# Performance work log

Hardware: AMD Instinct MI355X
Metric: run time of the kernel (lower is better)

The kernel has to match this reference:

```python
import jax, jax.numpy as jnp
import numpy as np

C = 60                 # channels
WINDOW_SIZES = [4, 8, 12]
SHIFTS = 4
BN_EPS = 1e-5


def setup_inputs() -> dict:
    key = jax.random.key(0)
    ks = jax.random.split(key, 4)
    s = 0.05
    return {
        "x": jax.random.normal(ks[0], (8, C, 288, 288), dtype=jnp.float32),
        # project_inp: Conv2d(C, 2C, k=1) + BatchNorm2d(2C) (inference form)
        "W_in": jax.random.normal(ks[1], (2 * C, C), dtype=jnp.float32) * s,
        "b_in": jnp.zeros((2 * C,), dtype=jnp.float32),
        "bn_gamma": jnp.ones((2 * C,), dtype=jnp.float32),
        "bn_beta": jnp.zeros((2 * C,), dtype=jnp.float32),
        "bn_mean": jax.random.normal(ks[2], (2 * C,), dtype=jnp.float32) * s,
        "bn_var": jnp.ones((2 * C,), dtype=jnp.float32),
        # project_out: Conv2d(C, C, k=1)
        "W_out": jax.random.normal(ks[3], (C, C), dtype=jnp.float32) * s,
        "b_out": jnp.zeros((C,), dtype=jnp.float32),
    }


def _window_self_attn(x_, wsize, shift):
    """One GMSA branch: roll -> window partition -> QQ^T softmax V -> merge -> unroll.
    x_ : [b, 2c, H, W] where first c channels are q, last c are v."""
    b, c2, H, W = x_.shape
    c = c2 // 2
    if shift > 0:
        x_ = jnp.roll(x_, shift=(-(wsize // 2), -(wsize // 2)), axis=(2, 3))
    nh, nw = H // wsize, W // wsize
    # 'b (qv c) (h dh) (w dw) -> qv (b h w) (dh dw) c'
    xw = x_.reshape(b, 2, c, nh, wsize, nw, wsize)
    xw = xw.transpose(1, 0, 3, 5, 4, 6, 2).reshape(2, b * nh * nw, wsize * wsize, c)
    q, v = xw[0], xw[1]                      # [n, p, c] with p = wsize*wsize
    atn = jax.nn.softmax(jnp.einsum("npc,nqc->npq", q, q), axis=-1)
    y = jnp.einsum("npq,nqc->npc", atn, v)
    # '(b h w) (dh dw) c -> b c (h dh) (w dw)'
    y = y.reshape(b, nh, nw, wsize, wsize, c).transpose(0, 5, 1, 3, 2, 4)
    y = y.reshape(b, c, H, W)
    if shift > 0:
        y = jnp.roll(y, shift=(wsize // 2, wsize // 2), axis=(2, 3))
    return y, atn


def reference(x, W_in, b_in, bn_gamma, bn_beta, bn_mean, bn_var, W_out, b_out):
    # 1x1 conv = channel matmul, then inference BatchNorm
    xp = jnp.einsum("oc,bchw->bohw", W_in, x) + b_in[None, :, None, None]
    inv = bn_gamma / jnp.sqrt(bn_var + BN_EPS)
    xp = xp * inv[None, :, None, None] + (bn_beta - bn_mean * inv)[None, :, None, None]
    split = 2 * C // 3  # = 40 per branch (q,v interleaved as 2x20)
    ys, atns = [], []
    off = 0
    for ws in WINDOW_SIZES:
        y_, a_ = _window_self_attn(xp[:, off:off + split], ws, SHIFTS)
        off += split
        ys.append(y_)
        atns.append(a_)
    y = jnp.concatenate(ys, axis=1)  # [b, C, H, W]
    y = jnp.einsum("oc,bchw->bohw", W_out, y) + b_out[None, :, None, None]
    return (y, atns[0], atns[1], atns[2])
```

## Files before the change

kernel.cpp:

```cpp
#include <hip/hip_runtime.h>


constexpr int HW = 288 * 288;
constexpr long long ATN0_OFF = 39813120LL;
constexpr long long ATN1_OFF = ATN0_OFF + 41472LL * 256;
constexpr long long ATN2_OFF = ATN1_OFF + 10368LL * 4096;

constexpr size_t YB_OFF = 0;
constexpr size_t WP_OFF = 79626240;
constexpr size_t BP_OFF = WP_OFF + 28800;
constexpr size_t XP_OFF = BP_OFF + 512;

typedef __attribute__((ext_vector_type(8))) short  bf16x8;
typedef __attribute__((ext_vector_type(4))) short  bf16x4;
typedef __attribute__((ext_vector_type(4))) float  f32x4;

__device__ __forceinline__ unsigned bfrnd(float f) {
    unsigned u = __float_as_uint(f);
    return (u + 0x7fffu + ((u >> 16) & 1u)) >> 16;
}
__device__ __forceinline__ unsigned bfpack(float a, float b) { return bfrnd(a) | (bfrnd(b) << 16); }

#if defined(__has_builtin)
#if __has_builtin(__builtin_amdgcn_mfma_f32_16x16x16bf16_1k)
#define HAVE_MFMA16 1
#endif
#endif

__device__ __forceinline__ f32x4 mfma16(bf16x4 a, bf16x4 b, f32x4 c) {
#ifdef HAVE_MFMA16
    return __builtin_amdgcn_mfma_f32_16x16x16bf16_1k(a, b, c, 0, 0, 0);
#else
    f32x4 d;
    asm("v_mfma_f32_16x16x16_bf16 %0, %1, %2, %3" : "=v"(d) : "v"(a), "v"(b), "v"(c));
    return d;
#endif
}

__device__ __forceinline__ f32x4 mfma32(bf16x8 a, bf16x8 b, f32x4 c) {
    return __builtin_amdgcn_mfma_f32_16x16x32_bf16(a, b, c, 0, 0, 0);
}

__global__ void prep_kernel(const float* __restrict__ W_in, const float* __restrict__ b_in,
                            const float* __restrict__ gamma, const float* __restrict__ beta,
                            const float* __restrict__ mean, const float* __restrict__ var,
                            float* __restrict__ Wp, float* __restrict__ bp) {
    int o = threadIdx.x;
    if (o < 120) {
        float inv = gamma[o] / sqrtf(var[o] + 1e-5f);
        for (int c = 0; c < 60; ++c) Wp[o * 60 + c] = W_in[o * 60 + c] * inv;
        bp[o] = b_in[o] * inv + beta[o] - mean[o] * inv;
    } else if (o < 128) {
        bp[o] = 0.f;
    }
}

__global__ __launch_bounds__(256, 3) void proj_in_kernel(const float* __restrict__ x,
                                                         const float* __restrict__ Wp,
                                                         const float* __restrict__ bp,
                                                         unsigned short* __restrict__ xp) {
    __shared__ __align__(16) unsigned short wq[128 * 64];
    __shared__ __align__(16) unsigned short ys[128 * 120];

    const int tid = threadIdx.x;
    const long long pixel0 = (long long)blockIdx.x * 128;
    const int b   = (int)(pixel0 / HW);
    const int hw0 = (int)(pixel0 % HW);

    for (int i = tid; i < 8192; i += 256) {
        const int row = i >> 6, ch = i & 63;
        wq[i] = (row < 120 && ch < 60) ? (unsigned short)bfrnd(Wp[row * 60 + ch]) : (unsigned short)0;
    }

    const int wave = tid >> 6, lane = tid & 63, lo = lane & 15, g = lane >> 4;

    uint4 xlo[2], xhi[2];
    #pragma unroll
    for (int mt2 = 0; mt2 < 2; ++mt2) {
        const int row = (wave * 2 + mt2) * 16 + lo;
        const float* xb = x + (long long)b * 60 * HW + hw0 + row;
        unsigned short tl[8], th[8];
        #pragma unroll
        for (int e = 0; e < 8; ++e) {
            const int cl = g * 8 + e;
            tl[e] = (unsigned short)bfrnd(xb[(long long)cl * HW]);
            const int ch = 32 + g * 8 + e;
            th[e] = (ch < 60) ? (unsigned short)bfrnd(xb[(long long)ch * HW]) : (unsigned short)0;
        }
        xlo[mt2] = *reinterpret_cast<const uint4*>(tl);
        xhi[mt2] = *reinterpret_cast<const uint4*>(th);
    }
    __syncthreads();

    #pragma unroll
    for (int n = 0; n < 8; ++n) {
        uint4 wfl = *reinterpret_cast<const uint4*>(&wq[(n * 16 + lo) * 64 + g * 8]);
        uint4 wfh = *reinterpret_cast<const uint4*>(&wq[(n * 16 + lo) * 64 + 32 + g * 8]);
        const int oc0 = n * 16 + 4 * g;
        const f32x4 bpv = *reinterpret_cast<const f32x4*>(&bp[oc0]);
        #pragma unroll
        for (int mt2 = 0; mt2 < 2; ++mt2) {
            f32x4 z = {0.f, 0.f, 0.f, 0.f};
            f32x4 acc = mfma32(*reinterpret_cast<bf16x8*>(&wfl),
                               *reinterpret_cast<bf16x8*>(&xlo[mt2]), z);
            acc = mfma32(*reinterpret_cast<bf16x8*>(&wfh),
                         *reinterpret_cast<bf16x8*>(&xhi[mt2]), acc);
            if (oc0 < 120) {
                const int pixel = (wave * 2 + mt2) * 16 + lo;
                uint2 t;
                t.x = bfpack(acc[0] + bpv[0], acc[1] + bpv[1]);
                t.y = bfpack(acc[2] + bpv[2], acc[3] + bpv[3]);
                *reinterpret_cast<uint2*>(&ys[pixel * 120 + oc0]) = t;
            }
        }
    }
    __syncthreads();

    for (int i = tid; i < 3 * 1280; i += 256) {
        const int br = i / 1280, j = i - br * 1280, p = j / 10, c = j - p * 10;
        const uint2 v = *reinterpret_cast<const uint2*>(&ys[p * 120 + br * 40 + c * 4]);
        reinterpret_cast<uint2*>(xp + ((long long)(b * 3 + br) * HW + hw0) * 40)[p * 10 + c] = v;
    }
}

template <int WS, int NWIN, int BLOCK, int WPW, int BRANCH, int MINW>
__launch_bounds__(BLOCK, MINW)
__global__ void branch_kernel(const unsigned short* __restrict__ xp,
                              unsigned short* __restrict__ ybuf,
                              float* __restrict__ atn) {
    constexpr int P    = WS * WS;
    constexpr int RT   = P / 16;
    constexpr int SH   = WS / 2;
    constexpr int NWND = 288 / WS;
    constexpr int RSTR = 56;
    constexpr int WAVES = BLOCK / 64;
    constexpr int WINS_PER_WAVE = (NWIN * WPW) / WAVES;

    __shared__ __align__(16) unsigned short qv[NWIN * P * RSTR];
    __shared__ __align__(16) unsigned short ys[NWIN * P * 20];

    const int tid = threadIdx.x;
    const int w0 = blockIdx.x * NWIN;

    for (int idx = tid; idx < NWIN * P * 5; idx += BLOCK) {
        const int wl  = idx / (P * 5);
        const int rem = idx - wl * (P * 5);
        const int pix = rem / 5;
        const int ck  = rem - pix * 5;
        const int w   = w0 + wl;
        const int b   = w / (NWND * NWND);
        const int r2  = w - b * (NWND * NWND);
        const int wi  = r2 / NWND;
        const int wj  = r2 - wi * NWND;
        const int gh  = (wi * WS + pix / WS + SH) % 288;
        const int gw  = (wj * WS + pix % WS + SH) % 288;
        const uint4 d = *reinterpret_cast<const uint4*>(
            xp + ((long long)(b * 3 + BRANCH) * HW + gh * 288 + gw) * 40 + ck * 8);
        *reinterpret_cast<uint4*>(&qv[(wl * P + pix) * RSTR + ck * 8]) = d;
    }
    __syncthreads();

    const int wave = tid >> 6;
    const int lane = tid & 63;
    const int lo   = lane & 15;
    const int g    = lane >> 4;

    for (int wk = 0; wk < WINS_PER_WAVE; ++wk) {
        const int wl   = (WPW == 1) ? (wave * WINS_PER_WAVE + wk) : (wave >> 1);
        const int half = (WPW == 1) ? 0 : (wave & 1);
        const int w    = w0 + wl;
        const unsigned short* wbase = qv + wl * P * RSTR;

        bf16x8 F[RT];
        #pragma unroll
        for (int t = 0; t < RT; ++t) {
            uint4 u = *reinterpret_cast<const uint4*>(&wbase[(16 * t + lo) * RSTR + g * 8]);
            if (g == 2) { u.z = 0; u.w = 0; }
            if (g == 3) { u.x = 0; u.y = 0; u.z = 0; u.w = 0; }
            F[t] = *reinterpret_cast<bf16x8*>(&u);
        }

        bf16x4 VB[RT][2];
        #pragma unroll
        for (int i = 0; i < RT; ++i) {
            #pragma unroll
            for (int ct = 0; ct < 2; ++ct) {
                const int c = ct * 16 + lo;
                bf16x4 vv;
                #pragma unroll
                for (int jj = 0; jj < 4; ++jj) {
                    const int row = 16 * i + 4 * g + jj;
                    vv[jj] = (c < 20) ? (short)wbase[row * RSTR + 20 + c] : (short)0;
                }
                VB[i][ct] = vv;
            }
        }

        const int jstart = (WPW == 1) ? 0 : (half * ((RT + 1) / 2));
        const int jend   = (WPW == 1) ? RT : ((half == 0) ? ((RT + 1) / 2) : RT);
        for (int j = jstart; j < jend; ++j) {
            f32x4 S[RT];
            #pragma unroll
            for (int i = 0; i < RT; ++i) {
                f32x4 z = {0.f, 0.f, 0.f, 0.f};
                S[i] = mfma32(F[i], F[j], z);
            }

            float m = S[0][0];
            #pragma unroll
            for (int i = 0; i < RT; ++i) {
                #pragma unroll
                for (int r = 0; r < 4; ++r) m = fmaxf(m, S[i][r]);
            }
            m = fmaxf(m, __shfl_xor(m, 16));
            m = fmaxf(m, __shfl_xor(m, 32));
            float sum = 0.f;
            #pragma unroll
            for (int i = 0; i < RT; ++i) {
                #pragma unroll
                for (int r = 0; r < 4; ++r) { float e = __expf(S[i][r] - m); S[i][r] = e; sum += e; }
            }
            sum += __shfl_xor(sum, 16);
            sum += __shfl_xor(sum, 32);
            const float inv = 1.0f / sum;
            #pragma unroll
            for (int i = 0; i < RT; ++i) {
                S[i][0] *= inv; S[i][1] *= inv; S[i][2] *= inv; S[i][3] *= inv;
            }

            float* arow = atn + ((long long)w * P + 16 * j + lo) * P + 4 * g;
            #pragma unroll
            for (int i = 0; i < RT; ++i)
                *reinterpret_cast<f32x4*>(arow + 16 * i) = S[i];

            f32x4 Y0 = {0.f, 0.f, 0.f, 0.f};
            f32x4 Y1 = {0.f, 0.f, 0.f, 0.f};
            #pragma unroll
            for (int i = 0; i < RT; ++i) {
                uint2 t2;
                t2.x = bfpack(S[i][0], S[i][1]);
                t2.y = bfpack(S[i][2], S[i][3]);
                bf16x4 pa = *reinterpret_cast<bf16x4*>(&t2);
                Y0 = mfma16(pa, VB[i][0], Y0);
                Y1 = mfma16(pa, VB[i][1], Y1);
            }

            unsigned short* ywp = ys + (wl * P + 16 * j + 4 * g) * 20;
            #pragma unroll
            for (int r = 0; r < 4; ++r) ywp[r * 20 + lo] = (unsigned short)bfrnd(Y0[r]);
            if (lo < 4) {
                #pragma unroll
                for (int r = 0; r < 4; ++r) ywp[r * 20 + 16 + lo] = (unsigned short)bfrnd(Y1[r]);
            }
        }
    }
    __syncthreads();

    for (int i = tid; i < NWIN * P * 5; i += BLOCK) {
        const int wl   = i / (P * 5);
        const int rem  = i - wl * (P * 5);
        const int pixr = rem / 5;
        const int c    = rem - pixr * 5;
        const int w2   = w0 + wl;
        const int b2   = w2 / (NWND * NWND);
        const int r2   = w2 - b2 * (NWND * NWND);
        const int wi2  = r2 / NWND;
        const int wj2  = r2 - wi2 * NWND;
        const int oh   = (wi2 * WS + pixr / WS + SH) % 288;
        const int ow   = (wj2 * WS + pixr % WS + SH) % 288;
        const uint2 v = *reinterpret_cast<const uint2*>(&ys[(wl * P + pixr) * 20 + c * 4]);
        *reinterpret_cast<uint2*>(ybuf + ((long long)(b2 * 3 + BRANCH) * HW + oh * 288 + ow) * 20 + c * 4) = v;
    }
}

__global__ __launch_bounds__(256, 2) void proj_out_kernel(const unsigned short* __restrict__ ybuf,
                                                          const float* __restrict__ W_out,
                                                          const float* __restrict__ bout,
                                                          float* __restrict__ out) {
    __shared__ __align__(16) unsigned short yh[128 * 72];
    __shared__ __align__(16) unsigned short wq[64 * 64];
    __shared__ __align__(16) float ost[60 * 132];

    const int tid = threadIdx.x;
    const long long pixel0 = (long long)blockIdx.x * 128;
    const int b   = (int)(pixel0 / HW);
    const int hw0 = (int)(pixel0 % HW);

    for (int i = tid; i < 4096; i += 256) {
        const int row = i >> 6, ch = i & 63;
        wq[i] = (row < 60 && ch < 60) ? (unsigned short)bfrnd(W_out[row * 60 + ch]) : (unsigned short)0;
    }

    for (int i = tid; i < 1920; i += 256) {
        const int br = i / 640, j = i - br * 640, p = j / 5, c = j - p * 5;
        const uint2 v = reinterpret_cast<const uint2*>(
            ybuf + ((long long)(b * 3 + br) * HW + hw0) * 20)[j];
        *reinterpret_cast<uint2*>(&yh[p * 72 + br * 20 + c * 4]) = v;
    }
    {
        const int p = tid >> 1, hh = tid & 1;
        *reinterpret_cast<uint2*>(&yh[p * 72 + 60 + hh * 4]) = make_uint2(0, 0);
    }
    __syncthreads();

    const int wave = tid >> 6, lane = tid & 63, lo = lane & 15, g = lane >> 4;

    uint4 alo[2], ahi[2];
    #pragma unroll
    for (int mt2 = 0; mt2 < 2; ++mt2) {
        const int row = (wave * 2 + mt2) * 16 + lo;
        alo[mt2] = *reinterpret_cast<const uint4*>(&yh[row * 72 + g * 8]);
        ahi[mt2] = *reinterpret_cast<const uint4*>(&yh[row * 72 + 32 + g * 8]);
    }

    #pragma unroll
    for (int n = 0; n < 4; ++n) {
        uint4 wfl = *reinterpret_cast<const uint4*>(&wq[(n * 16 + lo) * 64 + g * 8]);
        uint4 wfh = *reinterpret_cast<const uint4*>(&wq[(n * 16 + lo) * 64 + 32 + g * 8]);
        const int oc = n * 16 + lo;
        const float bo = (oc < 60) ? bout[oc] : 0.f;
        #pragma unroll
        for (int mt2 = 0; mt2 < 2; ++mt2) {
            f32x4 z = {0.f, 0.f, 0.f, 0.f};
            f32x4 acc = mfma32(*reinterpret_cast<bf16x8*>(&alo[mt2]),
                               *reinterpret_cast<bf16x8*>(&wfl), z);
            acc = mfma32(*reinterpret_cast<bf16x8*>(&ahi[mt2]),
                         *reinterpret_cast<bf16x8*>(&wfh), acc);
            if (oc < 60) {
                const int pcol = (wave * 2 + mt2) * 16 + 4 * g;
                #pragma unroll
                for (int r = 0; r < 4; ++r)
                    ost[oc * 132 + pcol + r] = acc[r] + bo;
            }
        }
    }
    __syncthreads();

    for (int i = tid; i < 1920; i += 256) {
        const int o = i >> 5, j = i & 31;
        const f32x4 v = *reinterpret_cast<const f32x4*>(&ost[o * 132 + j * 4]);
        *reinterpret_cast<f32x4*>(&out[((long long)b * 60 + o) * HW + hw0 + j * 4]) = v;
    }
}

extern "C" void kernel_launch(void* const* d_in, const int* in_sizes, int n_in,
                              void* d_out, int out_size, void* d_ws, size_t ws_size,
                              hipStream_t stream) {
    const float* x     = (const float*)d_in[0];
    const float* W_in  = (const float*)d_in[1];
    const float* b_in  = (const float*)d_in[2];
    const float* gamma = (const float*)d_in[3];
    const float* beta  = (const float*)d_in[4];
    const float* mean  = (const float*)d_in[5];
    const float* var   = (const float*)d_in[6];
    const float* Wout  = (const float*)d_in[7];
    const float* bout  = (const float*)d_in[8];
    float* out = (float*)d_out;

    char* wsb = (char*)d_ws;
    unsigned short* ybuf = (unsigned short*)(wsb + YB_OFF);
    float*          Wp   = (float*)(wsb + WP_OFF);
    float*          bp   = (float*)(wsb + BP_OFF);
    unsigned short* xp   = (unsigned short*)(wsb + XP_OFF);

    prep_kernel<<<1, 128, 0, stream>>>(W_in, b_in, gamma, beta, mean, var, Wp, bp);
    proj_in_kernel<<<5184, 256, 0, stream>>>(x, Wp, bp, xp);

    branch_kernel<4, 16, 256, 1, 0, 4><<<2592, 256, 0, stream>>>(xp, ybuf, out + ATN0_OFF);
    branch_kernel<8,  4, 256, 1, 1, 4><<<2592, 256, 0, stream>>>(xp, ybuf, out + ATN1_OFF);
    branch_kernel<12, 2, 256, 2, 2, 3><<<2304, 256, 0, stream>>>(xp, ybuf, out + ATN2_OFF);

    proj_out_kernel<<<5184, 256, 0, stream>>>(ybuf, Wout, bout, out);
}
```

Before: 511.4 us.

## Fold BN prep into proj_in and merge three branch kernels into one launch

Removes the separate single-block prep kernel by computing the BatchNorm scale and bias inside every proj_in block, with the weight scaling done while staging to shared memory. The three window-attention branch launches are combined into one kernel that picks its branch from the block index, using one shared-memory buffer sized for the largest branch. This cuts launch count and serialization gaps between kernels and lets the branches overlap. In exchange every block now runs the same register and LDS budget (occupancy hint 3) and the smaller branches allocate the largest branch's shared memory, which may lower their occupancy.

```diff
diff --git a/kernel.cpp b/kernel.cpp
--- a/kernel.cpp
+++ b/kernel.cpp
@@ -7,9 +7,7 @@
 constexpr long long ATN2_OFF = ATN1_OFF + 10368LL * 4096;
 
 constexpr size_t YB_OFF = 0;
-constexpr size_t WP_OFF = 79626240;
-constexpr size_t BP_OFF = WP_OFF + 28800;
-constexpr size_t XP_OFF = BP_OFF + 512;
+constexpr size_t XP_OFF = 79626240 + 28800 + 512;
 
 typedef __attribute__((ext_vector_type(8))) short  bf16x8;
 typedef __attribute__((ext_vector_type(4))) short  bf16x4;
@@ -41,35 +39,33 @@
     return __builtin_amdgcn_mfma_f32_16x16x32_bf16(a, b, c, 0, 0, 0);
 }
 
-__global__ void prep_kernel(const float* __restrict__ W_in, const float* __restrict__ b_in,
-                            const float* __restrict__ gamma, const float* __restrict__ beta,
-                            const float* __restrict__ mean, const float* __restrict__ var,
-                            float* __restrict__ Wp, float* __restrict__ bp) {
-    int o = threadIdx.x;
-    if (o < 120) {
-        float inv = gamma[o] / sqrtf(var[o] + 1e-5f);
-        for (int c = 0; c < 60; ++c) Wp[o * 60 + c] = W_in[o * 60 + c] * inv;
-        bp[o] = b_in[o] * inv + beta[o] - mean[o] * inv;
-    } else if (o < 128) {
-        bp[o] = 0.f;
-    }
-}
-
 __global__ __launch_bounds__(256, 3) void proj_in_kernel(const float* __restrict__ x,
-                                                         const float* __restrict__ Wp,
-                                                         const float* __restrict__ bp,
+                                                         const float* __restrict__ W_in,
+                                                         const float* __restrict__ b_in,
+                                                         const float* __restrict__ gamma,
+                                                         const float* __restrict__ beta,
+                                                         const float* __restrict__ mean,
+                                                         const float* __restrict__ var,
                                                          unsigned short* __restrict__ xp) {
     __shared__ __align__(16) unsigned short wq[128 * 64];
     __shared__ __align__(16) unsigned short ys[128 * 120];
+    __shared__ float invl[128];
+    __shared__ float bpl[128];
 
     const int tid = threadIdx.x;
     const long long pixel0 = (long long)blockIdx.x * 128;
     const int b   = (int)(pixel0 / HW);
     const int hw0 = (int)(pixel0 % HW);
 
-    for (int i = tid; i < 8192; i += 256) {
-        const int row = i >> 6, ch = i & 63;
-        wq[i] = (row < 120 && ch < 60) ? (unsigned short)bfrnd(Wp[row * 60 + ch]) : (unsigned short)0;
+    if (tid < 128) {
+        if (tid < 120) {
+            const float inv = gamma[tid] / sqrtf(var[tid] + 1e-5f);
+            invl[tid] = inv;
+            bpl[tid]  = b_in[tid] * inv + beta[tid] - mean[tid] * inv;
+        } else {
+            invl[tid] = 0.f;
+            bpl[tid]  = 0.f;
+        }
     }
 
     const int wave = tid >> 6, lane = tid & 63, lo = lane & 15, g = lane >> 4;
@@ -92,12 +88,19 @@
     }
     __syncthreads();
 
+    for (int i = tid; i < 8192; i += 256) {
+        const int row = i >> 6, ch = i & 63;
+        wq[i] = (row < 120 && ch < 60)
+              ? (unsigned short)bfrnd(W_in[row * 60 + ch] * invl[row]) : (unsigned short)0;
+    }
+    __syncthreads();
+
     #pragma unroll
     for (int n = 0; n < 8; ++n) {
         uint4 wfl = *reinterpret_cast<const uint4*>(&wq[(n * 16 + lo) * 64 + g * 8]);
         uint4 wfh = *reinterpret_cast<const uint4*>(&wq[(n * 16 + lo) * 64 + 32 + g * 8]);
         const int oc0 = n * 16 + 4 * g;
-        const f32x4 bpv = *reinterpret_cast<const f32x4*>(&bp[oc0]);
+        const f32x4 bpv = *reinterpret_cast<const f32x4*>(&bpl[oc0]);
         #pragma unroll
         for (int mt2 = 0; mt2 < 2; ++mt2) {
             f32x4 z = {0.f, 0.f, 0.f, 0.f};
@@ -123,11 +126,11 @@
     }
 }
 
-template <int WS, int NWIN, int BLOCK, int WPW, int BRANCH, int MINW>
-__launch_bounds__(BLOCK, MINW)
-__global__ void branch_kernel(const unsigned short* __restrict__ xp,
-                              unsigned short* __restrict__ ybuf,
-                              float* __restrict__ atn) {
+template <int WS, int NWIN, int BLOCK, int WPW, int BRANCH>
+__device__ __forceinline__ void branch_body(char* smem,
+                                            const unsigned short* __restrict__ xp,
+                                            unsigned short* __restrict__ ybuf,
+                                            float* __restrict__ atn, int blk) {
     constexpr int P    = WS * WS;
     constexpr int RT   = P / 16;
     constexpr int SH   = WS / 2;
@@ -136,11 +139,11 @@
     constexpr int WAVES = BLOCK / 64;
     constexpr int WINS_PER_WAVE = (NWIN * WPW) / WAVES;
 
-    __shared__ __align__(16) unsigned short qv[NWIN * P * RSTR];
-    __shared__ __align__(16) unsigned short ys[NWIN * P * 20];
+    unsigned short* qv = reinterpret_cast<unsigned short*>(smem);
+    unsigned short* ys = reinterpret_cast<unsigned short*>(smem) + NWIN * P * RSTR;
 
     const int tid = threadIdx.x;
-    const int w0 = blockIdx.x * NWIN;
+    const int w0 = blk * NWIN;
 
     for (int idx = tid; idx < NWIN * P * 5; idx += BLOCK) {
         const int wl  = idx / (P * 5);
@@ -273,6 +276,18 @@
     }
 }
 
+__global__ __launch_bounds__(256, 3) void branches_kernel(const unsigned short* __restrict__ xp,
+                                                          unsigned short* __restrict__ ybuf,
+                                                          float* __restrict__ atn0,
+                                                          float* __restrict__ atn1,
+                                                          float* __restrict__ atn2) {
+    __shared__ __align__(16) char smem[43776];
+    const int bid = blockIdx.x;
+    if (bid < 2592)       branch_body<4, 16, 256, 1, 0>(smem, xp, ybuf, atn0, bid);
+    else if (bid < 5184)  branch_body<8,  4, 256, 1, 1>(smem, xp, ybuf, atn1, bid - 2592);
+    else                  branch_body<12, 2, 256, 2, 2>(smem, xp, ybuf, atn2, bid - 5184);
+}
+
 __global__ __launch_bounds__(256, 2) void proj_out_kernel(const unsigned short* __restrict__ ybuf,
                                                           const float* __restrict__ W_out,
                                                           const float* __restrict__ bout,
@@ -359,16 +374,10 @@
 
     char* wsb = (char*)d_ws;
     unsigned short* ybuf = (unsigned short*)(wsb + YB_OFF);
-    float*          Wp   = (float*)(wsb + WP_OFF);
-    float*          bp   = (float*)(wsb + BP_OFF);
     unsigned short* xp   = (unsigned short*)(wsb + XP_OFF);
 
-    prep_kernel<<<1, 128, 0, stream>>>(W_in, b_in, gamma, beta, mean, var, Wp, bp);
-    proj_in_kernel<<<5184, 256, 0, stream>>>(x, Wp, bp, xp);
-
-    branch_kernel<4, 16, 256, 1, 0, 4><<<2592, 256, 0, stream>>>(xp, ybuf, out + ATN0_OFF);
-    branch_kernel<8,  4, 256, 1, 1, 4><<<2592, 256, 0, stream>>>(xp, ybuf, out + ATN1_OFF);
-    branch_kernel<12, 2, 256, 2, 2, 3><<<2304, 256, 0, stream>>>(xp, ybuf, out + ATN2_OFF);
-
+    proj_in_kernel<<<5184, 256, 0, stream>>>(x, W_in, b_in, gamma, beta, mean, var, xp);
+    branches_kernel<<<7488, 256, 0, stream>>>(xp, ybuf,
+                                              out + ATN0_OFF, out + ATN1_OFF, out + ATN2_OFF);
     proj_out_kernel<<<5184, 256, 0, stream>>>(ybuf, Wout, bout, out);
 }
```

Measured after the change: 521.8 us. 2.0% more time.
